# Optimization experiments

Hardware: AMD Instinct MI355X
Metric: run time of the kernel (lower is better)

Reference implementation:

```python
import jax, jax.numpy as jnp
import numpy as np

NU, NN, NS = 50000, 20000, 2000
D_IN, D_HID, D_OUT = 128, 128, 64
LRELU_SLOPE = 0.01  # torch F.leaky_relu default


def _edges(k, n_src, n_dst, e):
    k1, k2 = jax.random.split(k)
    return (jax.random.randint(k1, (e,), 0, n_src, dtype=jnp.int32),
            jax.random.randint(k2, (e,), 0, n_dst, dtype=jnp.int32))


def setup_inputs() -> dict:
    key = jax.random.key(0)
    ks = jax.random.split(key, 32)
    fs, fd = _edges(ks[0], NU, NU, 500000)
    ps, pd = _edges(ks[1], NU, NN, 300000)
    pbs, pbd = _edges(ks[2], NN, NU, 300000)
    us, ud = _edges(ks[3], NS, NN, 150000)
    ubs, ubd = _edges(ks[4], NN, NS, 150000)
    s = 0.05
    inp = {
        "x_user": jax.random.normal(ks[5], (NU, D_IN), jnp.float32),
        "x_news": jax.random.normal(ks[6], (NN, D_IN), jnp.float32),
        "x_source": jax.random.normal(ks[7], (NS, D_IN), jnp.float32),
        # stacked per-relation GraphConv params, order:
        # [follows, posts, posted_by, publishes, published_by]
        "W1": jax.random.normal(ks[8], (5, D_IN, D_HID), jnp.float32) * s,
        "b1": jnp.zeros((5, D_HID), jnp.float32),
        "W2": jax.random.normal(ks[9], (5, D_HID, D_HID), jnp.float32) * s,
        "b2": jnp.zeros((5, D_HID), jnp.float32),
        "Wu": jax.random.normal(ks[10], (D_HID, D_OUT), jnp.float32) * s,
        "bu": jnp.zeros((D_OUT,), jnp.float32),
        "Wn": jax.random.normal(ks[11], (D_HID, D_OUT), jnp.float32) * s,
        "bn": jnp.zeros((D_OUT,), jnp.float32),
        "Ws": jax.random.normal(ks[12], (D_HID, D_OUT), jnp.float32) * s,
        "bs": jnp.zeros((D_OUT,), jnp.float32),
        "follows_src": fs, "follows_dst": fd,
        "posts_src": ps, "posts_dst": pd,
        "postedby_src": pbs, "postedby_dst": pbd,
        "publishes_src": us, "publishes_dst": ud,
        "publishedby_src": ubs, "publishedby_dst": ubd,
    }
    return inp


def _gconv(x_src, src, dst, n_dst, W, b):
    """DGL GraphConv, norm='both': D_dst^-1/2 A D_src^-1/2 X W + b."""
    n_src = x_src.shape[0]
    ones = jnp.ones(src.shape[0], x_src.dtype)
    dout = jnp.clip(jax.ops.segment_sum(ones, src, num_segments=n_src), 1.0)
    din = jnp.clip(jax.ops.segment_sum(ones, dst, num_segments=n_dst), 1.0)
    h = (x_src * jax.lax.rsqrt(dout)[:, None]) @ W  # transform before gather
    agg = jax.ops.segment_sum(h[src], dst, num_segments=n_dst)
    return agg * jax.lax.rsqrt(din)[:, None] + b


def _hetero_layer(xu, xn, xs, E, W, b):
    # mean aggregation across relations sharing a dst type
    hu = 0.5 * (_gconv(xu, E["fs"], E["fd"], NU, W[0], b[0])
                + _gconv(xn, E["pbs"], E["pbd"], NU, W[2], b[2]))
    hn = 0.5 * (_gconv(xu, E["ps"], E["pd"], NN, W[1], b[1])
                + _gconv(xs, E["us"], E["ud"], NN, W[3], b[3]))
    hs = _gconv(xn, E["ubs"], E["ubd"], NS, W[4], b[4])
    return hu, hn, hs


def reference(x_user, x_news, x_source, W1, b1, W2, b2, Wu, bu, Wn, bn, Ws, bs,
              follows_src, follows_dst, posts_src, posts_dst,
              postedby_src, postedby_dst, publishes_src, publishes_dst,
              publishedby_src, publishedby_dst):
    E = {"fs": follows_src, "fd": follows_dst, "ps": posts_src, "pd": posts_dst,
         "pbs": postedby_src, "pbd": postedby_dst, "us": publishes_src,
         "ud": publishes_dst, "ubs": publishedby_src, "ubd": publishedby_dst}
    lrelu = lambda v: jax.nn.leaky_relu(v, LRELU_SLOPE)
    hu, hn, hs = _hetero_layer(x_user, x_news, x_source, E, W1, b1)
    hu, hn, hs = lrelu(hu), lrelu(hn), lrelu(hs)
    hu, hn, hs = _hetero_layer(hu, hn, hs, E, W2, b2)
    hu, hn, hs = lrelu(hu), lrelu(hn), lrelu(hs)
    ou = hu @ Wu + bu
    on = hn @ Wn + bn
    os_ = hs @ Ws + bs
    return (ou, on, os_, hu, hn, hs)
```

## Files before the change

### kernel.cpp

```cpp
#include <hip/hip_runtime.h>

#define LRELU 0.01f

static const int kNU = 50000, kNN = 20000, kNS = 2000;
static const int DOUT_OFF[5] = {0, 100000, 170000, 240000, 262000};
static const int DIN_OFF[5]  = {50000, 150000, 190000, 242000, 282000};
static const int RP_OFF[5]   = {0, 50001, 70002, 120003, 140004};
static const int CSR_OFF[5]  = {0, 500000, 800000, 1100000, 1250000};

using bf16x8 = __attribute__((ext_vector_type(8))) short;
using u16x8  = __attribute__((ext_vector_type(8))) unsigned short;
using f32x4  = __attribute__((ext_vector_type(4))) float;

__device__ __forceinline__ float bf2f(unsigned short u) {
  return __uint_as_float(((unsigned)u) << 16);
}
__device__ __forceinline__ unsigned short f2bf(float f) {
  unsigned u = __float_as_uint(f);
  u += 0x7FFFu + ((u >> 16) & 1u);
  return (unsigned short)(u >> 16);
}


struct HArgs { const int* esrc[5]; const int* edst[5]; int* pos; int* partial; };

__global__ __launch_bounds__(512) void k_hist(HArgs a) {
  __shared__ int hbin[8192];
  int bx = blockIdx.x;
  int t = threadIdx.x;
  if (bx < 336) {
    constexpr int DSTART[6] = {0, 112, 160, 272, 320, 336};
    constexpr int NDT[5] = {50000, 20000, 50000, 20000, 2000};
    constexpr int CS[5]  = {31250, 18750, 18750, 9375, 9375};
    constexpr int EE[5]  = {500000, 300000, 300000, 150000, 150000};
    constexpr int PB[5]  = {0, 800000, 1120000, 1920000, 2240000};
    constexpr int COFF[5] = {0, 500000, 800000, 1100000, 1250000};
    int r = 0;
    while (bx >= DSTART[r + 1]) ++r;
    int local = bx - DSTART[r];
    int g = local / 16, c = local % 16;
    int nd = NDT[r];
    int gbase = g * 8192;
    int gend = gbase + 8192 < nd ? gbase + 8192 : nd;
    const int* dst = a.edst[r];
    int* pos = a.pos + COFF[r];
    int elo = c * CS[r];
    int ehi = elo + CS[r] < EE[r] ? elo + CS[r] : EE[r];
    for (int j = t; j < 8192; j += 512) hbin[j] = 0;
    __syncthreads();
    int span = ehi - elo;
    int efull = elo + (span / 4096) * 4096;
    for (int b = elo + t; b < efull; b += 4096) {
      int d[8];
#pragma unroll
      for (int k = 0; k < 8; ++k) d[k] = dst[b + k * 512];
#pragma unroll
      for (int k = 0; k < 8; ++k)
        if (d[k] >= gbase && d[k] < gend)
          pos[b + k * 512] = atomicAdd(&hbin[d[k] - gbase], 1);
    }
    for (int e = efull + t; e < ehi; e += 512) {
      int d = dst[e];
      if (d >= gbase && d < gend) pos[e] = atomicAdd(&hbin[d - gbase], 1);
    }
    __syncthreads();
    int* out = a.partial + PB[r] + (size_t)c * nd + gbase;
    int nn = gend - gbase;
    for (int j = t; j < nn; j += 512) out[j] = hbin[j];
  } else {
    constexpr int OSTART[6] = {0, 112, 224, 272, 288, 336};
    constexpr int NST[5] = {50000, 50000, 20000, 2000, 20000};
    constexpr int CS[5]  = {31250, 18750, 18750, 9375, 9375};
    constexpr int EE[5]  = {500000, 300000, 300000, 150000, 150000};
    constexpr int PB[5]  = {2272000, 3072000, 3872000, 4192000, 4224000};
    int idx = bx - 336;
    int r = 0;
    while (idx >= OSTART[r + 1]) ++r;
    int local = idx - OSTART[r];
    int g = local / 16, c = local % 16;
    int ns = NST[r];
    int gbase = g * 8192;
    int gend = gbase + 8192 < ns ? gbase + 8192 : ns;
    const int* src = a.esrc[r];
    int elo = c * CS[r];
    int ehi = elo + CS[r] < EE[r] ? elo + CS[r] : EE[r];
    for (int j = t; j < 8192; j += 512) hbin[j] = 0;
    __syncthreads();
    int span = ehi - elo;
    int efull = elo + (span / 4096) * 4096;
    for (int b = elo + t; b < efull; b += 4096) {
      int s[8];
#pragma unroll
      for (int k = 0; k < 8; ++k) s[k] = src[b + k * 512];
#pragma unroll
      for (int k = 0; k < 8; ++k)
        if (s[k] >= gbase && s[k] < gend) atomicAdd(&hbin[s[k] - gbase], 1);
    }
    for (int e = efull + t; e < ehi; e += 512) {
      int s = src[e];
      if (s >= gbase && s < gend) atomicAdd(&hbin[s - gbase], 1);
    }
    __syncthreads();
    int* out = a.partial + PB[r] + (size_t)c * ns + gbase;
    int nn = gend - gbase;
    for (int j = t; j < nn; j += 512) out[j] = hbin[j];
  }
}


struct BArgs { int* partial; int* cnt; float* rs; };

__global__ __launch_bounds__(256) void k_scanB(BArgs a) {
  int bx = blockIdx.x;
  int t = threadIdx.x;
  if (bx < 555) {
    int i = bx * 256 + t;
    if (i >= 142000) return;
    constexpr int NDT[5] = {50000, 20000, 50000, 20000, 2000};
    constexpr int PB[5]  = {0, 800000, 1120000, 1920000, 2240000};
    constexpr int DOFF[5] = {50000, 150000, 190000, 242000, 282000};
    int r, d;
    if      (i < 50000)  { r = 0; d = i; }
    else if (i < 70000)  { r = 1; d = i - 50000; }
    else if (i < 120000) { r = 2; d = i - 70000; }
    else if (i < 140000) { r = 3; d = i - 120000; }
    else                 { r = 4; d = i - 140000; }
    int nd = NDT[r];
    int* p = a.partial + PB[r] + d;
    int run = 0;
#pragma unroll
    for (int c = 0; c < 16; ++c) {
      int v = p[(size_t)c * nd];
      p[(size_t)c * nd] = run;
      run += v;
    }
    a.cnt[DOFF[r] + d] = run;
    a.rs[DOFF[r] + d] = rsqrtf((float)(run > 1 ? run : 1));
  } else {
    int i = (bx - 555) * 256 + t;
    if (i >= 142000) return;
    constexpr int NST[5] = {50000, 50000, 20000, 2000, 20000};
    constexpr int PB[5]  = {2272000, 3072000, 3872000, 4192000, 4224000};
    constexpr int OOFF[5] = {0, 100000, 170000, 240000, 262000};
    int r, s;
    if      (i < 50000)  { r = 0; s = i; }
    else if (i < 100000) { r = 1; s = i - 50000; }
    else if (i < 120000) { r = 2; s = i - 100000; }
    else if (i < 122000) { r = 3; s = i - 120000; }
    else                 { r = 4; s = i - 122000; }
    int ns = NST[r];
    const int* p = a.partial + PB[r] + s;
    int sum = 0;
#pragma unroll
    for (int c = 0; c < 16; ++c) sum += p[(size_t)c * ns];
    a.rs[OOFF[r] + s] = rsqrtf((float)(sum > 1 ? sum : 1));
  }
}


struct S3Args { const int* cnt; int* rp; };

__global__ __launch_bounds__(256) void k_scan3(S3Args a) {
  constexpr int CSTART[6] = {0, 49, 69, 118, 138, 140};
  constexpr int NDT[5] = {50000, 20000, 50000, 20000, 2000};
  constexpr int DOFF[5] = {50000, 150000, 190000, 242000, 282000};
  constexpr int RPOFF[5] = {0, 50001, 70002, 120003, 140004};
  int bx = blockIdx.x, r = 0;
  while (bx >= CSTART[r + 1]) ++r;
  int chunk = bx - CSTART[r];
  int nch = CSTART[r + 1] - CSTART[r];
  int n = NDT[r];
  const int* cnt = a.cnt + DOFF[r];
  int* rp = a.rp + RPOFF[r];
  int t = threadIdx.x;
  __shared__ int sd[256];
  __shared__ int choff_sh;
  int lim = chunk * 1024;
  int pre = 0;
  for (int j = t; j < lim; j += 256) pre += cnt[j];
  sd[t] = pre;
  __syncthreads();
  for (int off = 128; off > 0; off >>= 1) {
    if (t < off) sd[t] += sd[t + off];
    __syncthreads();
  }
  if (t == 0) choff_sh = sd[0];
  __syncthreads();
  int idx0 = lim + t * 4;
  int v[4];
#pragma unroll
  for (int j = 0; j < 4; ++j) v[j] = (idx0 + j < n) ? cnt[idx0 + j] : 0;
  int tsum = v[0] + v[1] + v[2] + v[3];
  sd[t] = tsum;
  __syncthreads();
  for (int s = 1; s < 256; s <<= 1) {
    int add = (t >= s) ? sd[t - s] : 0;
    __syncthreads();
    sd[t] += add;
    __syncthreads();
  }
  int off = choff_sh + sd[t] - tsum;
#pragma unroll
  for (int j = 0; j < 4; ++j) {
    if (idx0 + j < n) rp[idx0 + j] = off;
    off += v[j];
  }
  if (chunk == nch - 1 && t == 255) rp[n] = choff_sh + sd[255];
}


struct TJob { const float* X; const float* W; unsigned short* Y; int M; };
struct PrepJob { const float* W0; const float* W128; unsigned short* hi;
                 unsigned short* lo; int NOUT; int lgK; int bstart; };
struct CXArgs { const int* esrc[5]; const int* edst[5]; const int* pos;
                const int* rp; const int* partial; int* csr;
                TJob tj[5]; PrepJob pj[6]; };

__device__ __forceinline__ void transform_body(const TJob& p, int bxl, int t) {
  int w = t >> 6, l = t & 63;
  int lo16 = l & 15, hi4 = l >> 4;
  int m0 = bxl * 64;
  int M = p.M;
  f32x4 acc[4][2] = {};
  for (int s = 0; s < 4; ++s) {
    int kbase = s * 32 + hi4 * 8;
    bf16x8 af[4];
#pragma unroll
    for (int mf = 0; mf < 4; ++mf) {
      int row = m0 + mf * 16 + lo16;
      row = row < M ? row : M - 1;
      const float* xr = &p.X[(size_t)row * 128 + kbase];
      float4 xa = *(const float4*)xr;
      float4 xb = *(const float4*)(xr + 4);
      af[mf][0] = (short)f2bf(xa.x); af[mf][1] = (short)f2bf(xa.y);
      af[mf][2] = (short)f2bf(xa.z); af[mf][3] = (short)f2bf(xa.w);
      af[mf][4] = (short)f2bf(xb.x); af[mf][5] = (short)f2bf(xb.y);
      af[mf][6] = (short)f2bf(xb.z); af[mf][7] = (short)f2bf(xb.w);
    }
#pragma unroll
    for (int nf = 0; nf < 2; ++nf) {
      int n = (w * 2 + nf) * 16 + lo16;
      bf16x8 bh, bl;
#pragma unroll
      for (int j = 0; j < 8; ++j) {
        float wv = p.W[(size_t)(kbase + j) * 128 + n];
        unsigned short h = f2bf(wv);
        bh[j] = (short)h;
        bl[j] = (short)f2bf(wv - bf2f(h));
      }
#pragma unroll
      for (int mf = 0; mf < 4; ++mf) {
        acc[mf][nf] = __builtin_amdgcn_mfma_f32_16x16x32_bf16(af[mf], bh, acc[mf][nf], 0, 0, 0);
        acc[mf][nf] = __builtin_amdgcn_mfma_f32_16x16x32_bf16(af[mf], bl, acc[mf][nf], 0, 0, 0);
      }
    }
  }
#pragma unroll
  for (int nf = 0; nf < 2; ++nf) {
    int col = (w * 2 + nf) * 16 + lo16;
#pragma unroll
    for (int mf = 0; mf < 4; ++mf) {
#pragma unroll
      for (int rr = 0; rr < 4; ++rr) {
        int row = m0 + mf * 16 + hi4 * 4 + rr;
        if (row < M) p.Y[(size_t)row * 128 + col] = f2bf(acc[mf][nf][rr]);
      }
    }
  }
}

__global__ __launch_bounds__(256) void k_buildCx(CXArgs a) {
  int bx = blockIdx.x;
  int t = threadIdx.x;
  int g = bx / 3, m = bx % 3;
  if (m == 0) {
    constexpr int ESTART[6] = {0, 489, 782, 1075, 1222, 1369};
    constexpr int NDT[5] = {50000, 20000, 50000, 20000, 2000};
    constexpr int CS[5]  = {31250, 18750, 18750, 9375, 9375};
    constexpr int EE[5]  = {500000, 300000, 300000, 150000, 150000};
    constexpr int PB[5]  = {0, 800000, 1120000, 1920000, 2240000};
    constexpr int RPOFF[5] = {0, 50001, 70002, 120003, 140004};
    constexpr int COFF[5] = {0, 500000, 800000, 1100000, 1250000};
    int idx = g;
    if (idx >= 1369) return;
    int r = 0;
    while (idx >= ESTART[r + 1]) ++r;
    int i0 = (idx - ESTART[r]) * 1024 + t;
    const int* edst = a.edst[r];
    const int* esrc = a.esrc[r];
    const int* pos = a.pos + COFF[r];
    const int* rp = a.rp + RPOFF[r];
    const int* pb = a.partial + PB[r];
    int* csr = a.csr + COFF[r];
    int E = EE[r], cs = CS[r], nd = NDT[r];
    int i[4], d[4];
    bool v[4];
#pragma unroll
    for (int k = 0; k < 4; ++k) {
      i[k] = i0 + k * 256;
      v[k] = i[k] < E;
      d[k] = v[k] ? edst[i[k]] : 0;
    }
    int slot[4];
#pragma unroll
    for (int k = 0; k < 4; ++k) {
      if (v[k]) {
        int c = i[k] / cs;
        slot[k] = rp[d[k]] + pb[(size_t)c * nd + d[k]] + pos[i[k]];
      }
    }
#pragma unroll
    for (int k = 0; k < 4; ++k)
      if (v[k]) csr[slot[k]] = esrc[i[k]];
  } else {
    int idx = g * 2 + (m - 1);
    if (idx < 2222) {
      constexpr int TSTART[6] = {0, 782, 1564, 1877, 1909, 2222};
      int r = 0;
      while (idx >= TSTART[r + 1]) ++r;
      transform_body(a.tj[r], idx - TSTART[r], t);
    } else if (idx < 2638) {
      int b = idx - 2222, ji = 0;
      while (ji < 5 && b >= a.pj[ji + 1].bstart) ++ji;
      PrepJob p = a.pj[ji];
      int eidx = (b - p.bstart) * 256 + t;
      int K = 1 << p.lgK;
      int n = eidx >> p.lgK, k = eidx & (K - 1);
      if (n >= p.NOUT) return;
      float w = (k < 128) ? p.W0[k * p.NOUT + n] : p.W128[(k - 128) * p.NOUT + n];
      unsigned short h = f2bf(w);
      float res = w - bf2f(h);
      p.hi[n * K + k] = h;
      p.lo[n * K + k] = f2bf(res);
    }
  }
}


#define GROW(vv, cc)                                                              \
  _Pragma("unroll") for (int q = 0; q < 8; ++q)                                   \
      acc[q] = fmaf(__uint_as_float(((unsigned)(unsigned short)vv[q]) << 16), cc, acc[q]);

__device__ __forceinline__ void gat_accum(const int* __restrict__ rp,
    const int* __restrict__ csr, const unsigned short* __restrict__ Y,
    const float* __restrict__ rso, int wid, int sub, float* acc) {
  int e0 = rp[wid], e1 = rp[wid + 1];
  for (int base = e0; base < e1; base += 16) {
    int m = e1 - base;
    if (m > 16) m = 16;
    int ei = base + (sub < m ? sub : 0);
    int se = csr[ei];
    float sc = rso[se];
    if (m == 16) {
      bf16x8 v[16];
#pragma unroll
      for (int j = 0; j < 16; ++j) {
        int sj = __shfl(se, j, 16);
        v[j] = *(const bf16x8*)&Y[(size_t)sj * 128 + sub * 8];
      }
#pragma unroll
      for (int j = 0; j < 16; ++j) {
        float cj = __shfl(sc, j, 16);
        GROW(v[j], cj)
      }
    } else {
      int j = 0;
      for (; j + 8 <= m; j += 8) {
        int s0 = __shfl(se, j, 16), s1 = __shfl(se, j + 1, 16);
        int s2 = __shfl(se, j + 2, 16), s3 = __shfl(se, j + 3, 16);
        int s4 = __shfl(se, j + 4, 16), s5 = __shfl(se, j + 5, 16);
        int s6 = __shfl(se, j + 6, 16), s7 = __shfl(se, j + 7, 16);
        float c0 = __shfl(sc, j, 16), c1 = __shfl(sc, j + 1, 16);
        float c2 = __shfl(sc, j + 2, 16), c3 = __shfl(sc, j + 3, 16);
        float c4 = __shfl(sc, j + 4, 16), c5 = __shfl(sc, j + 5, 16);
        float c6 = __shfl(sc, j + 6, 16), c7 = __shfl(sc, j + 7, 16);
        bf16x8 v0 = *(const bf16x8*)&Y[(size_t)s0 * 128 + sub * 8];
        bf16x8 v1 = *(const bf16x8*)&Y[(size_t)s1 * 128 + sub * 8];
        bf16x8 v2 = *(const bf16x8*)&Y[(size_t)s2 * 128 + sub * 8];
        bf16x8 v3 = *(const bf16x8*)&Y[(size_t)s3 * 128 + sub * 8];
        bf16x8 v4 = *(const bf16x8*)&Y[(size_t)s4 * 128 + sub * 8];
        bf16x8 v5 = *(const bf16x8*)&Y[(size_t)s5 * 128 + sub * 8];
        bf16x8 v6 = *(const bf16x8*)&Y[(size_t)s6 * 128 + sub * 8];
        bf16x8 v7 = *(const bf16x8*)&Y[(size_t)s7 * 128 + sub * 8];
        GROW(v0, c0) GROW(v1, c1) GROW(v2, c2) GROW(v3, c3)
        GROW(v4, c4) GROW(v5, c5) GROW(v6, c6) GROW(v7, c7)
      }
      for (; j < m; ++j) {
        int s0 = __shfl(se, j, 16);
        float c0 = __shfl(sc, j, 16);
        bf16x8 v0 = *(const bf16x8*)&Y[(size_t)s0 * 128 + sub * 8];
        GROW(v0, c0)
      }
    }
  }
}


struct G1Rel { const int* rp; const int* csr; const unsigned short* Y;
               const float* rso; const float* rsi; };
struct G1Args { G1Rel rel[5]; const float* b;
                unsigned short* hU; unsigned short* hN; unsigned short* hS; };

__global__ __launch_bounds__(256) void k_gather1(G1Args a) {
  int bx = blockIdx.x;
  int t = threadIdx.x;
  int sub = t & 15;
  float acc[8], tot[8];
#pragma unroll
  for (int q = 0; q < 8; ++q) acc[q] = 0.f;
  if (bx < 3125) {
    int wid = bx * 16 + (t >> 4);
    gat_accum(a.rel[0].rp, a.rel[0].csr, a.rel[0].Y, a.rel[0].rso, wid, sub, acc);
    float s0 = a.rel[0].rsi[wid];
#pragma unroll
    for (int q = 0; q < 8; ++q) { tot[q] = s0 * acc[q]; acc[q] = 0.f; }
    gat_accum(a.rel[2].rp, a.rel[2].csr, a.rel[2].Y, a.rel[2].rso, wid, sub, acc);
    float s2 = a.rel[2].rsi[wid];
    const float* b0 = a.b;
    const float* b2 = a.b + 2 * 128;
    u16x8 o;
#pragma unroll
    for (int q = 0; q < 8; ++q) {
      float v = 0.5f * (tot[q] + s2 * acc[q] + b0[sub * 8 + q] + b2[sub * 8 + q]);
      v = v >= 0.f ? v : LRELU * v;
      o[q] = f2bf(v);
    }
    *(u16x8*)&a.hU[(size_t)wid * 128 + sub * 8] = o;
  } else if (bx < 4375) {
    int wid = (bx - 3125) * 16 + (t >> 4);
    gat_accum(a.rel[1].rp, a.rel[1].csr, a.rel[1].Y, a.rel[1].rso, wid, sub, acc);
    float s1 = a.rel[1].rsi[wid];
#pragma unroll
    for (int q = 0; q < 8; ++q) { tot[q] = s1 * acc[q]; acc[q] = 0.f; }
    gat_accum(a.rel[3].rp, a.rel[3].csr, a.rel[3].Y, a.rel[3].rso, wid, sub, acc);
    float s3 = a.rel[3].rsi[wid];
    const float* b1v = a.b + 128;
    const float* b3 = a.b + 3 * 128;
    u16x8 o;
#pragma unroll
    for (int q = 0; q < 8; ++q) {
      float v = 0.5f * (tot[q] + s3 * acc[q] + b1v[sub * 8 + q] + b3[sub * 8 + q]);
      v = v >= 0.f ? v : LRELU * v;
      o[q] = f2bf(v);
    }
    *(u16x8*)&a.hN[(size_t)wid * 128 + sub * 8] = o;
  } else {
    int wid = (bx - 4375) * 16 + (t >> 4);
    gat_accum(a.rel[4].rp, a.rel[4].csr, a.rel[4].Y, a.rel[4].rso, wid, sub, acc);
    float s4 = a.rel[4].rsi[wid];
    const float* b4 = a.b + 4 * 128;
    u16x8 o;
#pragma unroll
    for (int q = 0; q < 8; ++q) {
      float v = s4 * acc[q] + b4[sub * 8 + q];
      v = v >= 0.f ? v : LRELU * v;
      o[q] = f2bf(v);
    }
    *(u16x8*)&a.hS[(size_t)wid * 128 + sub * 8] = o;
  }
}


struct RelG {
  const int* rp; const int* csr; const unsigned short* xb;
  const float* rso; const float* rsi;
  unsigned short* out; int stride; int ooff; int nd;
};
struct GArgs { RelG rel[5]; };

__global__ __launch_bounds__(256) void k_gather(GArgs a) {
  constexpr int GSTART[6] = {0, 3125, 4375, 7500, 8750, 8875};
  int bx = blockIdx.x, r = 0;
  while (bx >= GSTART[r + 1]) ++r;
  RelG g = a.rel[r];
  int t = threadIdx.x;
  int sub = t & 15;
  int wid = (bx - GSTART[r]) * 16 + (t >> 4);
  if (wid >= g.nd) return;
  float acc[8];
#pragma unroll
  for (int q = 0; q < 8; ++q) acc[q] = 0.f;
  gat_accum(g.rp, g.csr, g.xb, g.rso, wid, sub, acc);
  float si = g.rsi[wid];
  u16x8 o;
#pragma unroll
  for (int q = 0; q < 8; ++q) o[q] = f2bf(acc[q] * si);
  *(u16x8*)&g.out[(size_t)wid * g.stride + g.ooff + sub * 8] = o;
}


struct MJob { const unsigned short* A; const unsigned short* Wh; const unsigned short* Wl;
              const float* b0; const float* b1; float scale; int lrelu;
              float* H; int ldh; unsigned short* Hb; int M; int bstart; };
struct MArgs { MJob j[3]; };

template <int KCH, int NW>
__device__ __forceinline__ void mgemm_body(const MJob& p, int bxl) {
  constexpr int KP = KCH * 128;
  int t = threadIdx.x;
  int w = t >> 6, l = t & 63;
  int lo16 = l & 15, hi4 = l >> 4;
  int m0 = bxl * 64;
  int M = p.M;
  const unsigned short* A = p.A;
  f32x4 acc[4][NW] = {};
  for (int s = 0; s < KP / 32; ++s) {
    int kbase = s * 32 + hi4 * 8;
    bf16x8 af[4];
#pragma unroll
    for (int mf = 0; mf < 4; ++mf) {
      int row = m0 + mf * 16 + lo16;
      row = row < M ? row : M - 1;
      af[mf] = *(const bf16x8*)&A[(size_t)row * KP + kbase];
    }
#pragma unroll
    for (int nf = 0; nf < NW; ++nf) {
      int n = (w * NW + nf) * 16 + lo16;
      bf16x8 bh = *(const bf16x8*)&p.Wh[(size_t)n * KP + kbase];
      bf16x8 bl = *(const bf16x8*)&p.Wl[(size_t)n * KP + kbase];
#pragma unroll
      for (int mf = 0; mf < 4; ++mf) {
        acc[mf][nf] = __builtin_amdgcn_mfma_f32_16x16x32_bf16(af[mf], bh, acc[mf][nf], 0, 0, 0);
        acc[mf][nf] = __builtin_amdgcn_mfma_f32_16x16x32_bf16(af[mf], bl, acc[mf][nf], 0, 0, 0);
      }
    }
  }
#pragma unroll
  for (int nf = 0; nf < NW; ++nf) {
    int col = (w * NW + nf) * 16 + lo16;
    float bs = p.b0 ? p.b0[col] : 0.f;
    if (p.b1) bs += p.b1[col];
#pragma unroll
    for (int mf = 0; mf < 4; ++mf) {
#pragma unroll
      for (int rr = 0; rr < 4; ++rr) {
        int row = m0 + mf * 16 + hi4 * 4 + rr;
        if (row < M) {
          float o = p.scale * (acc[mf][nf][rr] + bs);
          if (p.lrelu) o = o >= 0.f ? o : LRELU * o;
          if (p.H) p.H[(size_t)row * p.ldh + col] = o;
          if (p.Hb) p.Hb[(size_t)row * p.ldh + col] = f2bf(o);
        }
      }
    }
  }
}

__global__ __launch_bounds__(256) void k_mgemm3(MArgs a) {
  int bx = blockIdx.x;
  if (bx < a.j[1].bstart)      mgemm_body<2, 2>(a.j[0], bx);
  else if (bx < a.j[2].bstart) mgemm_body<2, 2>(a.j[1], bx - a.j[1].bstart);
  else                         mgemm_body<1, 2>(a.j[2], bx - a.j[2].bstart);
}

__global__ __launch_bounds__(256) void k_proj3(MArgs a) {
  int bx = blockIdx.x;
  if (bx < a.j[1].bstart)      mgemm_body<1, 1>(a.j[0], bx);
  else if (bx < a.j[2].bstart) mgemm_body<1, 1>(a.j[1], bx - a.j[1].bstart);
  else                         mgemm_body<1, 1>(a.j[2], bx - a.j[2].bstart);
}


extern "C" void kernel_launch(void* const* d_in, const int* in_sizes, int n_in,
                              void* d_out, int out_size, void* d_ws, size_t ws_size,
                              hipStream_t stream) {
  const float* xu = (const float*)d_in[0];
  const float* xn = (const float*)d_in[1];
  const float* xs = (const float*)d_in[2];
  const float* W1 = (const float*)d_in[3];
  const float* b1 = (const float*)d_in[4];
  const float* W2 = (const float*)d_in[5];
  const float* b2 = (const float*)d_in[6];
  const float* Wu = (const float*)d_in[7];
  const float* bu = (const float*)d_in[8];
  const float* Wn = (const float*)d_in[9];
  const float* bn = (const float*)d_in[10];
  const float* Wsrc = (const float*)d_in[11];
  const float* bsrc = (const float*)d_in[12];
  const int* SRC[5] = {(const int*)d_in[13], (const int*)d_in[15], (const int*)d_in[17],
                       (const int*)d_in[19], (const int*)d_in[21]};
  const int* DST[5] = {(const int*)d_in[14], (const int*)d_in[16], (const int*)d_in[18],
                       (const int*)d_in[20], (const int*)d_in[22]};

  int* ws_i = (int*)d_ws;
  int* rp = ws_i;
  int* csr = ws_i + 142008;
  int* pos = ws_i + 1542008;
  int* cnt = ws_i + 2942328;
  float* rs = (float*)(ws_i + 3226328);
  unsigned short* wt = (unsigned short*)(rs + 284000);
  unsigned short* aggU = wt + 376832;
  unsigned short* aggN = aggU + 12800000;
  unsigned short* aggS = aggN + 5120000;
  unsigned short* xbU = aggS + 256000;
  unsigned short* xbN = xbU + 6400000;
  unsigned short* xbS = xbN + 2560000;

  unsigned short* L2U_h = wt + 163840, * L2U_l = wt + 196608;
  unsigned short* L2N_h = wt + 229376, * L2N_l = wt + 262144;
  unsigned short* L2S_h = wt + 294912, * L2S_l = wt + 311296;
  unsigned short* PU_h = wt + 327680, * PU_l = wt + 335872;
  unsigned short* PN_h = wt + 344064, * PN_l = wt + 352256;
  unsigned short* PS_h = wt + 360448, * PS_l = wt + 368640;

  float* outf = (float*)d_out;
  float* ou = outf;
  float* on = outf + 3200000;
  float* osrc = outf + 4480000;
  float* hu = outf + 4608000;
  float* hn = outf + 11008000;
  float* hs = outf + 13568000;

  int* partial = (int*)outf;

  unsigned short* Yb = (unsigned short*)(outf + 4608000);
  unsigned short* Y0 = Yb;
  unsigned short* Y1 = Y0 + 6400000;
  unsigned short* Y2a = Y1 + 6400000;
  unsigned short* Y3 = Y2a + 2560000;
  unsigned short* Y4 = Y3 + 256000;

  HArgs ha;
  for (int r = 0; r < 5; ++r) { ha.esrc[r] = SRC[r]; ha.edst[r] = DST[r]; }
  ha.pos = pos;
  ha.partial = partial;
  k_hist<<<672, 512, 0, stream>>>(ha);

  BArgs ba = {partial, cnt, rs};
  k_scanB<<<1110, 256, 0, stream>>>(ba);

  S3Args s3 = {cnt, rp};
  k_scan3<<<140, 256, 0, stream>>>(s3);

  CXArgs ca;
  for (int r = 0; r < 5; ++r) { ca.esrc[r] = SRC[r]; ca.edst[r] = DST[r]; }
  ca.pos = pos;
  ca.rp = rp;
  ca.partial = partial;
  ca.csr = csr;
  ca.tj[0] = {xu, W1 + 0 * 16384, Y0, kNU};
  ca.tj[1] = {xu, W1 + 1 * 16384, Y1, kNU};
  ca.tj[2] = {xn, W1 + 2 * 16384, Y2a, kNN};
  ca.tj[3] = {xs, W1 + 3 * 16384, Y3, kNS};
  ca.tj[4] = {xn, W1 + 4 * 16384, Y4, kNN};
  ca.pj[0] = {W2, W2 + 2 * 16384, L2U_h, L2U_l, 128, 8, 0};
  ca.pj[1] = {W2 + 16384, W2 + 3 * 16384, L2N_h, L2N_l, 128, 8, 128};
  ca.pj[2] = {W2 + 4 * 16384, nullptr, L2S_h, L2S_l, 128, 7, 256};
  ca.pj[3] = {Wu, nullptr, PU_h, PU_l, 64, 7, 320};
  ca.pj[4] = {Wn, nullptr, PN_h, PN_l, 64, 7, 352};
  ca.pj[5] = {Wsrc, nullptr, PS_h, PS_l, 64, 7, 384};
  k_buildCx<<<4107, 256, 0, stream>>>(ca);

  G1Args g1;
  const unsigned short* YT[5] = {Y0, Y1, Y2a, Y3, Y4};
  for (int r = 0; r < 5; ++r)
    g1.rel[r] = {rp + RP_OFF[r], csr + CSR_OFF[r], YT[r],
                 rs + DOUT_OFF[r], rs + DIN_OFF[r]};
  g1.b = b1;
  g1.hU = xbU; g1.hN = xbN; g1.hS = xbS;
  k_gather1<<<4500, 256, 0, stream>>>(g1);

  {
    const unsigned short* XIN[5] = {xbU, xbU, xbN, xbS, xbN};
    unsigned short* OUT[5] = {aggU, aggN, aggU, aggN, aggS};
    const int OSTR[5] = {256, 256, 256, 256, 128};
    const int OOFF[5] = {0, 0, 128, 128, 0};
    GArgs ga;
    for (int r = 0; r < 5; ++r)
      ga.rel[r] = {rp + RP_OFF[r], csr + CSR_OFF[r], XIN[r], rs + DOUT_OFF[r],
                   rs + DIN_OFF[r], OUT[r], OSTR[r], OOFF[r],
                   (r == 0 || r == 2) ? kNU : (r == 4 ? kNS : kNN)};
    k_gather<<<8875, 256, 0, stream>>>(ga);
    MArgs ma;
    ma.j[0] = {aggU, L2U_h, L2U_l, b2, b2 + 2 * 128, 0.5f, 1, hu, 128, xbU, kNU, 0};
    ma.j[1] = {aggN, L2N_h, L2N_l, b2 + 128, b2 + 3 * 128, 0.5f, 1, hn, 128, xbN, kNN, 782};
    ma.j[2] = {aggS, L2S_h, L2S_l, b2 + 4 * 128, nullptr, 1.0f, 1, hs, 128, xbS, kNS, 1095};
    k_mgemm3<<<1127, 256, 0, stream>>>(ma);
  }

  MArgs pm;
  pm.j[0] = {xbU, PU_h, PU_l, bu, nullptr, 1.0f, 0, ou, 64, nullptr, kNU, 0};
  pm.j[1] = {xbN, PN_h, PN_l, bn, nullptr, 1.0f, 0, on, 64, nullptr, kNN, 782};
  pm.j[2] = {xbS, PS_h, PS_l, bsrc, nullptr, 1.0f, 0, osrc, 64, nullptr, kNS, 1095};
  k_proj3<<<1127, 256, 0, stream>>>(pm);
}
```

Measured before the change: 322.2 us.

## Share X loads across paired first-layer transforms and fold row offsets into partials

The first-layer feature transforms are moved into their own kernel that runs first. Each X tile is loaded and converted once and multiplied by two weight matrices for relations that share a source type (user, news), so the block count drops from 2222 to 1127. The scan kernel now adds the row-pointer offset into the per-chunk partial counts, so the CSR build does one fewer random gather per edge. The cost is losing the earlier interleaving of the CSR scatter with the MFMA transform work inside one launch, and the scan kernel gains extra read-modify-write traffic on the partials.

```diff
diff --git a/kernel.cpp b/kernel.cpp
--- a/kernel.cpp
+++ b/kernel.cpp
@@ -158,13 +158,14 @@
 }
 
 
-struct S3Args { const int* cnt; int* rp; };
+struct S3Args { const int* cnt; int* rp; int* partial; };
 
 __global__ __launch_bounds__(256) void k_scan3(S3Args a) {
   constexpr int CSTART[6] = {0, 49, 69, 118, 138, 140};
   constexpr int NDT[5] = {50000, 20000, 50000, 20000, 2000};
   constexpr int DOFF[5] = {50000, 150000, 190000, 242000, 282000};
   constexpr int RPOFF[5] = {0, 50001, 70002, 120003, 140004};
+  constexpr int PB[5]  = {0, 800000, 1120000, 1920000, 2240000};
   int bx = blockIdx.x, r = 0;
   while (bx >= CSTART[r + 1]) ++r;
   int chunk = bx - CSTART[r];
@@ -200,140 +201,165 @@
     __syncthreads();
   }
   int off = choff_sh + sd[t] - tsum;
+  int st[4];
 #pragma unroll
   for (int j = 0; j < 4; ++j) {
+    st[j] = off;
     if (idx0 + j < n) rp[idx0 + j] = off;
     off += v[j];
   }
   if (chunk == nch - 1 && t == 255) rp[n] = choff_sh + sd[255];
-}
-
-
-struct TJob { const float* X; const float* W; unsigned short* Y; int M; };
+  int* pb = a.partial + PB[r];
+  for (int c = 0; c < 16; ++c) {
+    size_t base = (size_t)c * n;
+#pragma unroll
+    for (int j = 0; j < 4; ++j)
+      if (idx0 + j < n) pb[base + idx0 + j] += st[j];
+  }
+}
+
+
+struct T2Job { const float* X; const float* Wa; const float* Wb;
+               unsigned short* Ya; unsigned short* Yb; int M; };
 struct PrepJob { const float* W0; const float* W128; unsigned short* hi;
                  unsigned short* lo; int NOUT; int lgK; int bstart; };
-struct CXArgs { const int* esrc[5]; const int* edst[5]; const int* pos;
-                const int* rp; const int* partial; int* csr;
-                TJob tj[5]; PrepJob pj[6]; };
-
-__device__ __forceinline__ void transform_body(const TJob& p, int bxl, int t) {
-  int w = t >> 6, l = t & 63;
-  int lo16 = l & 15, hi4 = l >> 4;
-  int m0 = bxl * 64;
-  int M = p.M;
-  f32x4 acc[4][2] = {};
-  for (int s = 0; s < 4; ++s) {
-    int kbase = s * 32 + hi4 * 8;
-    bf16x8 af[4];
-#pragma unroll
-    for (int mf = 0; mf < 4; ++mf) {
-      int row = m0 + mf * 16 + lo16;
-      row = row < M ? row : M - 1;
-      const float* xr = &p.X[(size_t)row * 128 + kbase];
-      float4 xa = *(const float4*)xr;
-      float4 xb = *(const float4*)(xr + 4);
-      af[mf][0] = (short)f2bf(xa.x); af[mf][1] = (short)f2bf(xa.y);
-      af[mf][2] = (short)f2bf(xa.z); af[mf][3] = (short)f2bf(xa.w);
-      af[mf][4] = (short)f2bf(xb.x); af[mf][5] = (short)f2bf(xb.y);
-      af[mf][6] = (short)f2bf(xb.z); af[mf][7] = (short)f2bf(xb.w);
-    }
-#pragma unroll
-    for (int nf = 0; nf < 2; ++nf) {
-      int n = (w * 2 + nf) * 16 + lo16;
-      bf16x8 bh, bl;
-#pragma unroll
-      for (int j = 0; j < 8; ++j) {
-        float wv = p.W[(size_t)(kbase + j) * 128 + n];
-        unsigned short h = f2bf(wv);
-        bh[j] = (short)h;
-        bl[j] = (short)f2bf(wv - bf2f(h));
-      }
-#pragma unroll
-      for (int mf = 0; mf < 4; ++mf) {
-        acc[mf][nf] = __builtin_amdgcn_mfma_f32_16x16x32_bf16(af[mf], bh, acc[mf][nf], 0, 0, 0);
-        acc[mf][nf] = __builtin_amdgcn_mfma_f32_16x16x32_bf16(af[mf], bl, acc[mf][nf], 0, 0, 0);
-      }
-    }
-  }
-#pragma unroll
-  for (int nf = 0; nf < 2; ++nf) {
-    int col = (w * 2 + nf) * 16 + lo16;
-#pragma unroll
-    for (int mf = 0; mf < 4; ++mf) {
-#pragma unroll
-      for (int rr = 0; rr < 4; ++rr) {
-        int row = m0 + mf * 16 + hi4 * 4 + rr;
-        if (row < M) p.Y[(size_t)row * 128 + col] = f2bf(acc[mf][nf][rr]);
-      }
-    }
-  }
-}
-
-__global__ __launch_bounds__(256) void k_buildCx(CXArgs a) {
+struct TArgs { T2Job j[3]; PrepJob pj[6]; };
+
+__global__ __launch_bounds__(256) void k_trans(TArgs a) {
   int bx = blockIdx.x;
   int t = threadIdx.x;
-  int g = bx / 3, m = bx % 3;
-  if (m == 0) {
-    constexpr int ESTART[6] = {0, 489, 782, 1075, 1222, 1369};
-    constexpr int NDT[5] = {50000, 20000, 50000, 20000, 2000};
-    constexpr int CS[5]  = {31250, 18750, 18750, 9375, 9375};
-    constexpr int EE[5]  = {500000, 300000, 300000, 150000, 150000};
-    constexpr int PB[5]  = {0, 800000, 1120000, 1920000, 2240000};
-    constexpr int RPOFF[5] = {0, 50001, 70002, 120003, 140004};
-    constexpr int COFF[5] = {0, 500000, 800000, 1100000, 1250000};
-    int idx = g;
-    if (idx >= 1369) return;
-    int r = 0;
-    while (idx >= ESTART[r + 1]) ++r;
-    int i0 = (idx - ESTART[r]) * 1024 + t;
-    const int* edst = a.edst[r];
-    const int* esrc = a.esrc[r];
-    const int* pos = a.pos + COFF[r];
-    const int* rp = a.rp + RPOFF[r];
-    const int* pb = a.partial + PB[r];
-    int* csr = a.csr + COFF[r];
-    int E = EE[r], cs = CS[r], nd = NDT[r];
-    int i[4], d[4];
-    bool v[4];
-#pragma unroll
-    for (int k = 0; k < 4; ++k) {
-      i[k] = i0 + k * 256;
-      v[k] = i[k] < E;
-      d[k] = v[k] ? edst[i[k]] : 0;
-    }
-    int slot[4];
-#pragma unroll
-    for (int k = 0; k < 4; ++k) {
-      if (v[k]) {
-        int c = i[k] / cs;
-        slot[k] = rp[d[k]] + pb[(size_t)c * nd + d[k]] + pos[i[k]];
-      }
-    }
-#pragma unroll
-    for (int k = 0; k < 4; ++k)
-      if (v[k]) csr[slot[k]] = esrc[i[k]];
+  if (bx < 1127) {
+    int ji, bxl;
+    if (bx < 782)       { ji = 0; bxl = bx; }
+    else if (bx < 1095) { ji = 1; bxl = bx - 782; }
+    else                { ji = 2; bxl = bx - 1095; }
+    const T2Job& p = a.j[ji];
+    int w = t >> 6, l = t & 63;
+    int lo16 = l & 15, hi4 = l >> 4;
+    int m0 = bxl * 64;
+    int M = p.M;
+    bool hasB = p.Wb != nullptr;
+    f32x4 accA[4][2] = {};
+    f32x4 accB[4][2] = {};
+    for (int s = 0; s < 4; ++s) {
+      int kbase = s * 32 + hi4 * 8;
+      bf16x8 af[4];
+#pragma unroll
+      for (int mf = 0; mf < 4; ++mf) {
+        int row = m0 + mf * 16 + lo16;
+        row = row < M ? row : M - 1;
+        const float* xr = &p.X[(size_t)row * 128 + kbase];
+        float4 xa = *(const float4*)xr;
+        float4 xb = *(const float4*)(xr + 4);
+        af[mf][0] = (short)f2bf(xa.x); af[mf][1] = (short)f2bf(xa.y);
+        af[mf][2] = (short)f2bf(xa.z); af[mf][3] = (short)f2bf(xa.w);
+        af[mf][4] = (short)f2bf(xb.x); af[mf][5] = (short)f2bf(xb.y);
+        af[mf][6] = (short)f2bf(xb.z); af[mf][7] = (short)f2bf(xb.w);
+      }
+#pragma unroll
+      for (int nf = 0; nf < 2; ++nf) {
+        int n = (w * 2 + nf) * 16 + lo16;
+        bf16x8 bh, bl;
+#pragma unroll
+        for (int j = 0; j < 8; ++j) {
+          float wv = p.Wa[(size_t)(kbase + j) * 128 + n];
+          unsigned short h = f2bf(wv);
+          bh[j] = (short)h;
+          bl[j] = (short)f2bf(wv - bf2f(h));
+        }
+#pragma unroll
+        for (int mf = 0; mf < 4; ++mf) {
+          accA[mf][nf] = __builtin_amdgcn_mfma_f32_16x16x32_bf16(af[mf], bh, accA[mf][nf], 0, 0, 0);
+          accA[mf][nf] = __builtin_amdgcn_mfma_f32_16x16x32_bf16(af[mf], bl, accA[mf][nf], 0, 0, 0);
+        }
+        if (hasB) {
+#pragma unroll
+          for (int j = 0; j < 8; ++j) {
+            float wv = p.Wb[(size_t)(kbase + j) * 128 + n];
+            unsigned short h = f2bf(wv);
+            bh[j] = (short)h;
+            bl[j] = (short)f2bf(wv - bf2f(h));
+          }
+#pragma unroll
+          for (int mf = 0; mf < 4; ++mf) {
+            accB[mf][nf] = __builtin_amdgcn_mfma_f32_16x16x32_bf16(af[mf], bh, accB[mf][nf], 0, 0, 0);
+            accB[mf][nf] = __builtin_amdgcn_mfma_f32_16x16x32_bf16(af[mf], bl, accB[mf][nf], 0, 0, 0);
+          }
+        }
+      }
+    }
+#pragma unroll
+    for (int nf = 0; nf < 2; ++nf) {
+      int col = (w * 2 + nf) * 16 + lo16;
+#pragma unroll
+      for (int mf = 0; mf < 4; ++mf) {
+#pragma unroll
+        for (int rr = 0; rr < 4; ++rr) {
+          int row = m0 + mf * 16 + hi4 * 4 + rr;
+          if (row < M) {
+            p.Ya[(size_t)row * 128 + col] = f2bf(accA[mf][nf][rr]);
+            if (hasB) p.Yb[(size_t)row * 128 + col] = f2bf(accB[mf][nf][rr]);
+          }
+        }
+      }
+    }
   } else {
-    int idx = g * 2 + (m - 1);
-    if (idx < 2222) {
-      constexpr int TSTART[6] = {0, 782, 1564, 1877, 1909, 2222};
-      int r = 0;
-      while (idx >= TSTART[r + 1]) ++r;
-      transform_body(a.tj[r], idx - TSTART[r], t);
-    } else if (idx < 2638) {
-      int b = idx - 2222, ji = 0;
-      while (ji < 5 && b >= a.pj[ji + 1].bstart) ++ji;
-      PrepJob p = a.pj[ji];
-      int eidx = (b - p.bstart) * 256 + t;
-      int K = 1 << p.lgK;
-      int n = eidx >> p.lgK, k = eidx & (K - 1);
-      if (n >= p.NOUT) return;
-      float w = (k < 128) ? p.W0[k * p.NOUT + n] : p.W128[(k - 128) * p.NOUT + n];
-      unsigned short h = f2bf(w);
-      float res = w - bf2f(h);
-      p.hi[n * K + k] = h;
-      p.lo[n * K + k] = f2bf(res);
-    }
-  }
+    int b = bx - 1127, ji = 0;
+    while (ji < 5 && b >= a.pj[ji + 1].bstart) ++ji;
+    PrepJob p = a.pj[ji];
+    int eidx = (b - p.bstart) * 256 + t;
+    int K = 1 << p.lgK;
+    int n = eidx >> p.lgK, k = eidx & (K - 1);
+    if (n >= p.NOUT) return;
+    float w = (k < 128) ? p.W0[k * p.NOUT + n] : p.W128[(k - 128) * p.NOUT + n];
+    unsigned short h = f2bf(w);
+    float res = w - bf2f(h);
+    p.hi[n * K + k] = h;
+    p.lo[n * K + k] = f2bf(res);
+  }
+}
+
+
+struct CArgs { const int* esrc[5]; const int* edst[5]; const int* pos;
+               const int* partial; int* csr; };
+
+__global__ __launch_bounds__(256) void k_buildC(CArgs a) {
+  constexpr int ESTART[6] = {0, 489, 782, 1075, 1222, 1369};
+  constexpr int NDT[5] = {50000, 20000, 50000, 20000, 2000};
+  constexpr int CS[5]  = {31250, 18750, 18750, 9375, 9375};
+  constexpr int EE[5]  = {500000, 300000, 300000, 150000, 150000};
+  constexpr int PB[5]  = {0, 800000, 1120000, 1920000, 2240000};
+  constexpr int COFF[5] = {0, 500000, 800000, 1100000, 1250000};
+  int bx = blockIdx.x;
+  int t = threadIdx.x;
+  int r = 0;
+  while (bx >= ESTART[r + 1]) ++r;
+  int i0 = (bx - ESTART[r]) * 1024 + t;
+  const int* edst = a.edst[r];
+  const int* esrc = a.esrc[r];
+  const int* pos = a.pos + COFF[r];
+  const int* pb = a.partial + PB[r];
+  int* csr = a.csr + COFF[r];
+  int E = EE[r], cs = CS[r], nd = NDT[r];
+  int i[4], d[4];
+  bool v[4];
+#pragma unroll
+  for (int k = 0; k < 4; ++k) {
+    i[k] = i0 + k * 256;
+    v[k] = i[k] < E;
+    d[k] = v[k] ? edst[i[k]] : 0;
+  }
+  int slot[4];
+#pragma unroll
+  for (int k = 0; k < 4; ++k) {
+    if (v[k]) {
+      int c = i[k] / cs;
+      slot[k] = pb[(size_t)c * nd + d[k]] + pos[i[k]];
+    }
+  }
+#pragma unroll
+  for (int k = 0; k < 4; ++k)
+    if (v[k]) csr[slot[k]] = esrc[i[k]];
 }
 
 
@@ -620,6 +646,18 @@
   unsigned short* Y3 = Y2a + 2560000;
   unsigned short* Y4 = Y3 + 256000;
 
+  TArgs ta;
+  ta.j[0] = {xu, W1 + 0 * 16384, W1 + 1 * 16384, Y0, Y1, kNU};
+  ta.j[1] = {xn, W1 + 2 * 16384, W1 + 4 * 16384, Y2a, Y4, kNN};
+  ta.j[2] = {xs, W1 + 3 * 16384, nullptr, Y3, nullptr, kNS};
+  ta.pj[0] = {W2, W2 + 2 * 16384, L2U_h, L2U_l, 128, 8, 0};
+  ta.pj[1] = {W2 + 16384, W2 + 3 * 16384, L2N_h, L2N_l, 128, 8, 128};
+  ta.pj[2] = {W2 + 4 * 16384, nullptr, L2S_h, L2S_l, 128, 7, 256};
+  ta.pj[3] = {Wu, nullptr, PU_h, PU_l, 64, 7, 320};
+  ta.pj[4] = {Wn, nullptr, PN_h, PN_l, 64, 7, 352};
+  ta.pj[5] = {Wsrc, nullptr, PS_h, PS_l, 64, 7, 384};
+  k_trans<<<1543, 256, 0, stream>>>(ta);
+
   HArgs ha;
   for (int r = 0; r < 5; ++r) { ha.esrc[r] = SRC[r]; ha.edst[r] = DST[r]; }
   ha.pos = pos;
@@ -629,27 +667,15 @@
   BArgs ba = {partial, cnt, rs};
   k_scanB<<<1110, 256, 0, stream>>>(ba);
 
-  S3Args s3 = {cnt, rp};
+  S3Args s3 = {cnt, rp, partial};
   k_scan3<<<140, 256, 0, stream>>>(s3);
 
-  CXArgs ca;
+  CArgs ca;
   for (int r = 0; r < 5; ++r) { ca.esrc[r] = SRC[r]; ca.edst[r] = DST[r]; }
   ca.pos = pos;
-  ca.rp = rp;
   ca.partial = partial;
   ca.csr = csr;
-  ca.tj[0] = {xu, W1 + 0 * 16384, Y0, kNU};
-  ca.tj[1] = {xu, W1 + 1 * 16384, Y1, kNU};
-  ca.tj[2] = {xn, W1 + 2 * 16384, Y2a, kNN};
-  ca.tj[3] = {xs, W1 + 3 * 16384, Y3, kNS};
-  ca.tj[4] = {xn, W1 + 4 * 16384, Y4, kNN};
-  ca.pj[0] = {W2, W2 + 2 * 16384, L2U_h, L2U_l, 128, 8, 0};
-  ca.pj[1] = {W2 + 16384, W2 + 3 * 16384, L2N_h, L2N_l, 128, 8, 128};
-  ca.pj[2] = {W2 + 4 * 16384, nullptr, L2S_h, L2S_l, 128, 7, 256};
-  ca.pj[3] = {Wu, nullptr, PU_h, PU_l, 64, 7, 320};
-  ca.pj[4] = {Wn, nullptr, PN_h, PN_l, 64, 7, 352};
-  ca.pj[5] = {Wsrc, nullptr, PS_h, PS_l, 64, 7, 384};
-  k_buildCx<<<4107, 256, 0, stream>>>(ca);
+  k_buildC<<<1369, 256, 0, stream>>>(ca);
 
   G1Args g1;
   const unsigned short* YT[5] = {Y0, Y1, Y2a, Y3, Y4};
```

Measured after the change: 339.5 us. 5.4% more time.

## Fuse layer-2 neighbor gather into GEMM via LDS-staged aggregated tile

Applied to the files above, without the earlier changes.

Replaces the separate layer-2 gather kernel and the aggregated-feature GEMM kernel with one kernel. Each 512-thread block gathers both relations for 64 destination rows into a swizzled shared-memory tile, then runs the MFMA GEMM directly from LDS. This removes the round trip of the bf16 aggregate buffers through global memory and one launch. In exchange it uses a larger LDS footprint, fewer blocks, and gather and GEMM phases that no longer overlap across kernels. It also writes layer-2 bf16 outputs to a separate buffer, because the gather now reads the layer-1 features while the same kernel writes its results.

```diff
diff --git a/kernel.cpp b/kernel.cpp
--- a/kernel.cpp
+++ b/kernel.cpp
@@ -461,31 +461,98 @@
 }
 
 
-struct RelG {
-  const int* rp; const int* csr; const unsigned short* xb;
-  const float* rso; const float* rsi;
-  unsigned short* out; int stride; int ooff; int nd;
+struct GMJob {
+  const int* rpA; const int* csrA; const unsigned short* YA;
+  const float* rsoA; const float* rsiA;
+  const int* rpB; const int* csrB; const unsigned short* YB;
+  const float* rsoB; const float* rsiB;
+  const unsigned short* Wh; const unsigned short* Wl;
+  const float* b0; const float* b1; float scale;
+  float* H; unsigned short* Hb; int M; int KP;
 };
-struct GArgs { RelG rel[5]; };
-
-__global__ __launch_bounds__(256) void k_gather(GArgs a) {
-  constexpr int GSTART[6] = {0, 3125, 4375, 7500, 8750, 8875};
-  int bx = blockIdx.x, r = 0;
-  while (bx >= GSTART[r + 1]) ++r;
-  RelG g = a.rel[r];
+struct GMArgs { GMJob j[3]; };
+
+__global__ __launch_bounds__(512) void k_gmm(GMArgs a) {
+  __shared__ unsigned short As[64 * 256];
+  int bx = blockIdx.x;
+  int ji, bxl;
+  if (bx < 782)       { ji = 0; bxl = bx; }
+  else if (bx < 1095) { ji = 1; bxl = bx - 782; }
+  else                { ji = 2; bxl = bx - 1095; }
+  const GMJob& p = a.j[ji];
   int t = threadIdx.x;
+  int m0 = bxl * 64;
+  char* asb = (char*)As;
   int sub = t & 15;
-  int wid = (bx - GSTART[r]) * 16 + (t >> 4);
-  if (wid >= g.nd) return;
-  float acc[8];
-#pragma unroll
-  for (int q = 0; q < 8; ++q) acc[q] = 0.f;
-  gat_accum(g.rp, g.csr, g.xb, g.rso, wid, sub, acc);
-  float si = g.rsi[wid];
-  u16x8 o;
-#pragma unroll
-  for (int q = 0; q < 8; ++q) o[q] = f2bf(acc[q] * si);
-  *(u16x8*)&g.out[(size_t)wid * g.stride + g.ooff + sub * 8] = o;
+  int rowloc = t >> 4;
+  for (int half = 0; half < 2; ++half) {
+    int rl = rowloc + half * 32;
+    int wid = m0 + rl;
+    bool ok = wid < p.M;
+    {
+      float acc[8];
+#pragma unroll
+      for (int q = 0; q < 8; ++q) acc[q] = 0.f;
+      float si = 0.f;
+      if (ok) { gat_accum(p.rpA, p.csrA, p.YA, p.rsoA, wid, sub, acc); si = p.rsiA[wid]; }
+      u16x8 o;
+#pragma unroll
+      for (int q = 0; q < 8; ++q) o[q] = f2bf(acc[q] * si);
+      int cb = sub * 16;
+      *(u16x8*)(asb + rl * 512 + (cb ^ ((rl & 7) << 4))) = o;
+    }
+    if (p.rpB) {
+      float acc[8];
+#pragma unroll
+      for (int q = 0; q < 8; ++q) acc[q] = 0.f;
+      float si = 0.f;
+      if (ok) { gat_accum(p.rpB, p.csrB, p.YB, p.rsoB, wid, sub, acc); si = p.rsiB[wid]; }
+      u16x8 o;
+#pragma unroll
+      for (int q = 0; q < 8; ++q) o[q] = f2bf(acc[q] * si);
+      int cb = 256 + sub * 16;
+      *(u16x8*)(asb + rl * 512 + (cb ^ ((rl & 7) << 4))) = o;
+    }
+  }
+  __syncthreads();
+  int w = t >> 6, l = t & 63;
+  int lo16 = l & 15, hi4 = l >> 4;
+  int KP = p.KP;
+  f32x4 acc[4] = {};
+  for (int s = 0; s < KP / 32; ++s) {
+    int kbase = s * 32 + hi4 * 8;
+    int cb = kbase * 2;
+    bf16x8 af[4];
+#pragma unroll
+    for (int mf = 0; mf < 4; ++mf) {
+      int row = mf * 16 + lo16;
+      af[mf] = *(const bf16x8*)(asb + row * 512 + (cb ^ ((row & 7) << 4)));
+    }
+    int n = w * 16 + lo16;
+    bf16x8 bh = *(const bf16x8*)&p.Wh[(size_t)n * KP + kbase];
+    bf16x8 bl = *(const bf16x8*)&p.Wl[(size_t)n * KP + kbase];
+#pragma unroll
+    for (int mf = 0; mf < 4; ++mf) {
+      acc[mf] = __builtin_amdgcn_mfma_f32_16x16x32_bf16(af[mf], bh, acc[mf], 0, 0, 0);
+      acc[mf] = __builtin_amdgcn_mfma_f32_16x16x32_bf16(af[mf], bl, acc[mf], 0, 0, 0);
+    }
+  }
+  int col = w * 16 + lo16;
+  float bs = p.b0[col];
+  if (p.b1) bs += p.b1[col];
+#pragma unroll
+  for (int mf = 0; mf < 4; ++mf) {
+#pragma unroll
+    for (int rr = 0; rr < 4; ++rr) {
+      int row = m0 + mf * 16 + hi4 * 4 + rr;
+      if (row < p.M) {
+        float o = p.scale * (acc[mf][rr] + bs);
+        o = o >= 0.f ? o : LRELU * o;
+        p.H[(size_t)row * 128 + col] = o;
+        p.Hb[(size_t)row * 128 + col] = f2bf(o);
+      }
+    }
+  }
 }
 
 
@@ -544,13 +611,6 @@
       }
     }
   }
-}
-
-__global__ __launch_bounds__(256) void k_mgemm3(MArgs a) {
-  int bx = blockIdx.x;
-  if (bx < a.j[1].bstart)      mgemm_body<2, 2>(a.j[0], bx);
-  else if (bx < a.j[2].bstart) mgemm_body<2, 2>(a.j[1], bx - a.j[1].bstart);
-  else                         mgemm_body<1, 2>(a.j[2], bx - a.j[2].bstart);
 }
 
 __global__ __launch_bounds__(256) void k_proj3(MArgs a) {
@@ -589,10 +649,10 @@
   int* cnt = ws_i + 2942328;
   float* rs = (float*)(ws_i + 3226328);
   unsigned short* wt = (unsigned short*)(rs + 284000);
-  unsigned short* aggU = wt + 376832;
-  unsigned short* aggN = aggU + 12800000;
-  unsigned short* aggS = aggN + 5120000;
-  unsigned short* xbU = aggS + 256000;
+  unsigned short* h2bU = wt + 376832;
+  unsigned short* h2bN = h2bU + 6400000;
+  unsigned short* h2bS = h2bN + 2560000;
+  unsigned short* xbU = wt + 376832 + 18176000;
   unsigned short* xbN = xbU + 6400000;
   unsigned short* xbS = xbN + 2560000;
 
@@ -660,27 +720,21 @@
   g1.hU = xbU; g1.hN = xbN; g1.hS = xbS;
   k_gather1<<<4500, 256, 0, stream>>>(g1);
 
-  {
-    const unsigned short* XIN[5] = {xbU, xbU, xbN, xbS, xbN};
-    unsigned short* OUT[5] = {aggU, aggN, aggU, aggN, aggS};
-    const int OSTR[5] = {256, 256, 256, 256, 128};
-    const int OOFF[5] = {0, 0, 128, 128, 0};
-    GArgs ga;
-    for (int r = 0; r < 5; ++r)
-      ga.rel[r] = {rp + RP_OFF[r], csr + CSR_OFF[r], XIN[r], rs + DOUT_OFF[r],
-                   rs + DIN_OFF[r], OUT[r], OSTR[r], OOFF[r],
-                   (r == 0 || r == 2) ? kNU : (r == 4 ? kNS : kNN)};
-    k_gather<<<8875, 256, 0, stream>>>(ga);
-    MArgs ma;
-    ma.j[0] = {aggU, L2U_h, L2U_l, b2, b2 + 2 * 128, 0.5f, 1, hu, 128, xbU, kNU, 0};
-    ma.j[1] = {aggN, L2N_h, L2N_l, b2 + 128, b2 + 3 * 128, 0.5f, 1, hn, 128, xbN, kNN, 782};
-    ma.j[2] = {aggS, L2S_h, L2S_l, b2 + 4 * 128, nullptr, 1.0f, 1, hs, 128, xbS, kNS, 1095};
-    k_mgemm3<<<1127, 256, 0, stream>>>(ma);
-  }
+  GMArgs gm;
+  gm.j[0] = {rp + RP_OFF[0], csr + CSR_OFF[0], xbU, rs + DOUT_OFF[0], rs + DIN_OFF[0],
+             rp + RP_OFF[2], csr + CSR_OFF[2], xbN, rs + DOUT_OFF[2], rs + DIN_OFF[2],
+             L2U_h, L2U_l, b2, b2 + 2 * 128, 0.5f, hu, h2bU, kNU, 256};
+  gm.j[1] = {rp + RP_OFF[1], csr + CSR_OFF[1], xbU, rs + DOUT_OFF[1], rs + DIN_OFF[1],
+             rp + RP_OFF[3], csr + CSR_OFF[3], xbS, rs + DOUT_OFF[3], rs + DIN_OFF[3],
+             L2N_h, L2N_l, b2 + 128, b2 + 3 * 128, 0.5f, hn, h2bN, kNN, 256};
+  gm.j[2] = {rp + RP_OFF[4], csr + CSR_OFF[4], xbN, rs + DOUT_OFF[4], rs + DIN_OFF[4],
+             nullptr, nullptr, nullptr, nullptr, nullptr,
+             L2S_h, L2S_l, b2 + 4 * 128, nullptr, 1.0f, hs, h2bS, kNS, 128};
+  k_gmm<<<1127, 512, 0, stream>>>(gm);
 
   MArgs pm;
-  pm.j[0] = {xbU, PU_h, PU_l, bu, nullptr, 1.0f, 0, ou, 64, nullptr, kNU, 0};
-  pm.j[1] = {xbN, PN_h, PN_l, bn, nullptr, 1.0f, 0, on, 64, nullptr, kNN, 782};
-  pm.j[2] = {xbS, PS_h, PS_l, bsrc, nullptr, 1.0f, 0, osrc, 64, nullptr, kNS, 1095};
+  pm.j[0] = {h2bU, PU_h, PU_l, bu, nullptr, 1.0f, 0, ou, 64, nullptr, kNU, 0};
+  pm.j[1] = {h2bN, PN_h, PN_l, bn, nullptr, 1.0f, 0, on, 64, nullptr, kNN, 782};
+  pm.j[2] = {h2bS, PS_h, PS_l, bsrc, nullptr, 1.0f, 0, osrc, 64, nullptr, kNS, 1095};
   k_proj3<<<1127, 256, 0, stream>>>(pm);
 }
```

Result: no change. 319.1 us (-1.0%).
